# Kernel tuning notes

Hardware: AMD Instinct MI355X
Metric: run time of the kernel (lower is better)

## Reference

```python
import jax, jax.numpy as jnp
import numpy as np

P = 16  # patch side

def setup_inputs() -> dict:
    key = jax.random.key(0)
    k1, k2, k3, k4, k5 = jax.random.split(key, 5)
    B, H, W_img, C = 32, 512, 512, 3
    hidden = 256
    n = (H // P) * (W_img // P)
    x = jax.random.normal(k1, (B, H, W_img, C), dtype=jnp.float32)
    W = jax.random.normal(k2, (P * P * C, hidden), dtype=jnp.float32) * 0.02
    b = jax.random.normal(k3, (hidden,), dtype=jnp.float32) * 0.02
    cls_token = jax.random.normal(k4, (B, 1, hidden), dtype=jnp.float32)
    pos_embedding = jax.random.normal(k5, (B, n + 1, hidden), dtype=jnp.float32) * 0.02
    return {"x": x, "W": W, "b": b, "cls_token": cls_token, "pos_embedding": pos_embedding}

def _patchify(x):
    # (B,H,W,C) -> (B, n, P*P*C); patch index = col + (H/P)*row, flatten order (p,p,c)
    B, H, W_img, C = x.shape
    gh, gw = H // P, W_img // P
    x = x.reshape(B, gh, P, gw, P, C)
    x = x.transpose(0, 1, 3, 2, 4, 5)  # (B, gh, gw, P, P, C)
    return x.reshape(B, gh * gw, P * P * C)

def reference(x, W, b, cls_token, pos_embedding):
    patches = _patchify(x)                       # (B, n, P*P*C)
    proj = jnp.einsum('bnd,dh->bnh', patches, W) + b  # (B, n, hidden)
    out = jnp.concatenate([cls_token, proj], axis=1) + pos_embedding  # (B, n+1, hidden)
    return out
```

## Files before the change

kernel.cpp:

```cpp
#include <hip/hip_runtime.h>

#define PSZ 16
#define BATCH 32
#define IMGH 512
#define IMGW 512
#define CH 3
#define NPATCH 1024
#define M_TOT (BATCH*NPATCH)
#define K_TOT 768
#define N_TOT 256
#define ROWSTRIDE (IMGW*CH)
#define IMGSTRIDE (IMGH*IMGW*CH)

#define BM 64
#define BN 128
#define BK 64
#define KPAD 72
#define NKIT (K_TOT/BK)

typedef __bf16 bf16_t;
typedef bf16_t bf16x8 __attribute__((ext_vector_type(8)));
typedef bf16_t bf16x4 __attribute__((ext_vector_type(4)));
typedef float f32x4 __attribute__((ext_vector_type(4)));

__global__ void prep_w(const float* __restrict__ Wsrc,
                       bf16_t* __restrict__ wth, bf16_t* __restrict__ wtl) {
    __shared__ float tile[32][33];
    const int d0 = blockIdx.x * 32;
    const int h0 = blockIdx.y * 32;
    const int tid = threadIdx.x;
#pragma unroll
    for (int i = 0; i < 4; ++i) {
        int idx = tid + i * 256;
        int r = idx >> 5, c = idx & 31;
        tile[r][c] = Wsrc[(d0 + r) * N_TOT + h0 + c];
    }
    __syncthreads();
#pragma unroll
    for (int i = 0; i < 4; ++i) {
        int idx = tid + i * 256;
        int r = idx >> 5, c = idx & 31;
        float v = tile[c][r];
        bf16_t h = (bf16_t)v;
        bf16_t l = (bf16_t)(v - (float)h);
        size_t o = (size_t)(h0 + r) * K_TOT + d0 + c;
        wth[o] = h;
        wtl[o] = l;
    }
}

__global__ void cls_add(const float* __restrict__ cls, const float* __restrict__ pos,
                        float* __restrict__ out) {
    int i = blockIdx.x * 256 + threadIdx.x;
    int b = i >> 8, h = i & 255;
    size_t o = (size_t)b * (NPATCH + 1) * N_TOT + h;
    out[o] = cls[i] + pos[o];
}

__global__ __launch_bounds__(256, 2)
void patch_gemm(const float* __restrict__ x,
                const bf16_t* __restrict__ wth, const bf16_t* __restrict__ wtl,
                const float* __restrict__ bias, const float* __restrict__ pos,
                float* __restrict__ out) {
    __shared__ bf16_t Ah[BM * KPAD];
    __shared__ bf16_t Al[BM * KPAD];
    __shared__ bf16_t Bh[BN * KPAD];
    __shared__ bf16_t Bl[BN * KPAD];

    const int bid = blockIdx.x;
    const int xcd = bid & 7, kk = bid >> 3;
    const int t = xcd * 128 + kk;
    const int mtile = t >> 1;
    const int ntile = t & 1;

    const int tid = threadIdx.x;
    const int lane = tid & 63;
    const int wid = tid >> 6;
    const int wr = wid >> 1, wc = wid & 1;

    const int m0 = mtile * BM;
    const int n0 = ntile * BN;

    f32x4 acc[2][4] = {};

    const int l15 = lane & 15;
    const int kgrp = (lane >> 4) << 3;

    for (int kit = 0; kit < NKIT; ++kit) {
#pragma unroll
        for (int i = 0; i < 4; ++i) {
            int f = tid + i * 256;
            int row = f >> 4;
            int kl = (f & 15) << 2;
            int pm = m0 + row;
            int b = pm >> 10, pid = pm & 1023;
            int gr = pid >> 5, gc = pid & 31;
            int d = kit * BK + kl;
            int prow = d / 48;
            int poff = d % 48;
            const float* src = x + (size_t)b * IMGSTRIDE
                               + (gr * PSZ + prow) * ROWSTRIDE + gc * (PSZ * CH) + poff;
            float4 v = *(const float4*)src;
            bf16x4 hv, lv;
            hv[0] = (bf16_t)v.x; lv[0] = (bf16_t)(v.x - (float)hv[0]);
            hv[1] = (bf16_t)v.y; lv[1] = (bf16_t)(v.y - (float)hv[1]);
            hv[2] = (bf16_t)v.z; lv[2] = (bf16_t)(v.z - (float)hv[2]);
            hv[3] = (bf16_t)v.w; lv[3] = (bf16_t)(v.w - (float)hv[3]);
            int o = row * KPAD + kl;
            *reinterpret_cast<bf16x4*>(&Ah[o]) = hv;
            *reinterpret_cast<bf16x4*>(&Al[o]) = lv;
        }
#pragma unroll
        for (int i = 0; i < 4; ++i) {
            int f = tid + i * 256;
            int row = f >> 3;
            int kl = (f & 7) << 3;
            size_t g = (size_t)(n0 + row) * K_TOT + kit * BK + kl;
            int o = row * KPAD + kl;
            *reinterpret_cast<bf16x8*>(&Bh[o]) = *reinterpret_cast<const bf16x8*>(&wth[g]);
            *reinterpret_cast<bf16x8*>(&Bl[o]) = *reinterpret_cast<const bf16x8*>(&wtl[g]);
        }
        __syncthreads();

#pragma unroll
        for (int ks = 0; ks < 2; ++ks) {
            const int kb = ks * 32 + kgrp;
            bf16x8 afh[2], afl[2];
#pragma unroll
            for (int ar = 0; ar < 2; ++ar) {
                int o = (wr * 32 + ar * 16 + l15) * KPAD + kb;
                afh[ar] = *reinterpret_cast<const bf16x8*>(&Ah[o]);
                afl[ar] = *reinterpret_cast<const bf16x8*>(&Al[o]);
            }
            bf16x8 bfh[4], bfl[4];
#pragma unroll
            for (int bc = 0; bc < 4; ++bc) {
                int o = (wc * 64 + bc * 16 + l15) * KPAD + kb;
                bfh[bc] = *reinterpret_cast<const bf16x8*>(&Bh[o]);
                bfl[bc] = *reinterpret_cast<const bf16x8*>(&Bl[o]);
            }
#pragma unroll
            for (int ar = 0; ar < 2; ++ar)
#pragma unroll
                for (int bc = 0; bc < 4; ++bc) {
                    acc[ar][bc] = __builtin_amdgcn_mfma_f32_16x16x32_bf16(afh[ar], bfh[bc], acc[ar][bc], 0, 0, 0);
                    acc[ar][bc] = __builtin_amdgcn_mfma_f32_16x16x32_bf16(afh[ar], bfl[bc], acc[ar][bc], 0, 0, 0);
                    acc[ar][bc] = __builtin_amdgcn_mfma_f32_16x16x32_bf16(afl[ar], bfh[bc], acc[ar][bc], 0, 0, 0);
                }
        }
        __syncthreads();
    }

    const int colbase = n0 + wc * 64;
    float bvals[4];
#pragma unroll
    for (int bc = 0; bc < 4; ++bc) bvals[bc] = bias[colbase + bc * 16 + l15];

#pragma unroll
    for (int ar = 0; ar < 2; ++ar) {
        int rbase = m0 + wr * 32 + ar * 16 + ((lane >> 4) << 2);
#pragma unroll
        for (int j = 0; j < 4; ++j) {
            int pm = rbase + j;
            int b = pm >> 10, p = pm & 1023;
            size_t orow = (size_t)(b * (NPATCH + 1) + 1 + p) * N_TOT;
#pragma unroll
            for (int bc = 0; bc < 4; ++bc) {
                int col = colbase + bc * 16 + l15;
                out[orow + col] = acc[ar][bc][j] + bvals[bc] + pos[orow + col];
            }
        }
    }
}

extern "C" void kernel_launch(void* const* d_in, const int* in_sizes, int n_in,
                              void* d_out, int out_size, void* d_ws, size_t ws_size,
                              hipStream_t stream) {
    const float* x    = (const float*)d_in[0];
    const float* W    = (const float*)d_in[1];
    const float* bias = (const float*)d_in[2];
    const float* cls  = (const float*)d_in[3];
    const float* pos  = (const float*)d_in[4];
    float* out = (float*)d_out;

    bf16_t* wth = (bf16_t*)d_ws;
    bf16_t* wtl = wth + (size_t)K_TOT * N_TOT;

    prep_w<<<dim3(24, 8), 256, 0, stream>>>(W, wth, wtl);
    cls_add<<<32, 256, 0, stream>>>(cls, pos, out);
    patch_gemm<<<1024, 256, 0, stream>>>(x, wth, wtl, bias, pos, out);
}
```

Measured before the change: 210.2 us.

## Prepack weights in MFMA fragment order, double-buffer A tiles, drop B LDS staging

Weight prep now writes the hi/lo bf16 weights directly in the per-lane MFMA fragment order. The GEMM then loads B fragments straight from global memory (L2-resident) instead of staging them through shared memory. The A tile (patch pixels split into hi/lo bf16) is double-buffered in LDS, with the next tile's global loads issued before the MFMAs and the conversion stores after them, so there is one barrier per iteration. The smaller LDS footprint allows raising launch bounds to 4 blocks per CU. The trade-off is more global/L2 traffic for B, since each wave re-reads its fragments, plus some register pressure from the prefetched float4 values.

Measured after the change: 215.3 us. +2.4%, slower.

```diff
diff --git a/kernel.cpp b/kernel.cpp
--- a/kernel.cpp
+++ b/kernel.cpp
@@ -6,7 +6,6 @@
 #define IMGW 512
 #define CH 3
 #define NPATCH 1024
-#define M_TOT (BATCH*NPATCH)
 #define K_TOT 768
 #define N_TOT 256
 #define ROWSTRIDE (IMGW*CH)
@@ -20,33 +19,28 @@
 
 typedef __bf16 bf16_t;
 typedef bf16_t bf16x8 __attribute__((ext_vector_type(8)));
-typedef bf16_t bf16x4 __attribute__((ext_vector_type(4)));
 typedef float f32x4 __attribute__((ext_vector_type(4)));
 
 __global__ void prep_w(const float* __restrict__ Wsrc,
-                       bf16_t* __restrict__ wth, bf16_t* __restrict__ wtl) {
-    __shared__ float tile[32][33];
-    const int d0 = blockIdx.x * 32;
-    const int h0 = blockIdx.y * 32;
-    const int tid = threadIdx.x;
-#pragma unroll
-    for (int i = 0; i < 4; ++i) {
-        int idx = tid + i * 256;
-        int r = idx >> 5, c = idx & 31;
-        tile[r][c] = Wsrc[(d0 + r) * N_TOT + h0 + c];
-    }
-    __syncthreads();
-#pragma unroll
-    for (int i = 0; i < 4; ++i) {
-        int idx = tid + i * 256;
-        int r = idx >> 5, c = idx & 31;
-        float v = tile[c][r];
-        bf16_t h = (bf16_t)v;
-        bf16_t l = (bf16_t)(v - (float)h);
-        size_t o = (size_t)(h0 + r) * K_TOT + d0 + c;
-        wth[o] = h;
-        wtl[o] = l;
-    }
+                       bf16x8* __restrict__ wfh, bf16x8* __restrict__ wfl) {
+    int t = blockIdx.x * 256 + threadIdx.x;
+    int lane = t & 63;
+    int ks = (t >> 6) & 1;
+    int rest = t >> 7;
+    int kit = rest % 12;
+    int bcg = rest / 12;
+    int col = bcg * 16 + (lane & 15);
+    int kbase = kit * 64 + ks * 32 + ((lane >> 4) << 3);
+    bf16x8 h, l;
+#pragma unroll
+    for (int e = 0; e < 8; ++e) {
+        float v = Wsrc[(size_t)(kbase + e) * N_TOT + col];
+        bf16_t hh = (bf16_t)v;
+        h[e] = hh;
+        l[e] = (bf16_t)(v - (float)hh);
+    }
+    wfh[t] = h;
+    wfl[t] = l;
 }
 
 __global__ void cls_add(const float* __restrict__ cls, const float* __restrict__ pos,
@@ -57,19 +51,16 @@
     out[o] = cls[i] + pos[o];
 }
 
-__global__ __launch_bounds__(256, 2)
+__global__ __launch_bounds__(256, 4)
 void patch_gemm(const float* __restrict__ x,
-                const bf16_t* __restrict__ wth, const bf16_t* __restrict__ wtl,
+                const bf16x8* __restrict__ wfh, const bf16x8* __restrict__ wfl,
                 const float* __restrict__ bias, const float* __restrict__ pos,
                 float* __restrict__ out) {
-    __shared__ bf16_t Ah[BM * KPAD];
-    __shared__ bf16_t Al[BM * KPAD];
-    __shared__ bf16_t Bh[BN * KPAD];
-    __shared__ bf16_t Bl[BN * KPAD];
+    __shared__ bf16_t Ah[2][BM * KPAD];
+    __shared__ bf16_t Al[2][BM * KPAD];
 
     const int bid = blockIdx.x;
-    const int xcd = bid & 7, kk = bid >> 3;
-    const int t = xcd * 128 + kk;
+    const int t = (bid & 7) * 128 + (bid >> 3);
     const int mtile = t >> 1;
     const int ntile = t & 1;
 
@@ -85,59 +76,81 @@
 
     const int l15 = lane & 15;
     const int kgrp = (lane >> 4) << 3;
-
+    const int bcg0 = ntile * 8 + wc * 4;
+
+    const int rowb = tid >> 3;
+    const int kl8 = (tid & 7) << 3;
+    const float* srcbase[2];
+#pragma unroll
+    for (int i = 0; i < 2; ++i) {
+        int row = rowb + 32 * i;
+        int pm = m0 + row;
+        int b = pm >> 10, pid = pm & 1023;
+        int gr = pid >> 5, gc = pid & 31;
+        srcbase[i] = x + (size_t)b * IMGSTRIDE + (gr * PSZ) * ROWSTRIDE + gc * (PSZ * CH);
+    }
+
+#define LOADA(KIT, P0, P1, P2, P3)                                        \
+    {                                                                      \
+        int d = (KIT) * BK + kl8;                                          \
+        int prow = d / 48, poff = d % 48;                                  \
+        const float* s0 = srcbase[0] + prow * ROWSTRIDE + poff;            \
+        const float* s1 = srcbase[1] + prow * ROWSTRIDE + poff;            \
+        P0 = *(const float4*)s0;  P1 = *(const float4*)(s0 + 4);           \
+        P2 = *(const float4*)s1;  P3 = *(const float4*)(s1 + 4);           \
+    }
+
+#define CVTSTORE(BUF, P0, P1, P2, P3)                                      \
+    {                                                                      \
+        bf16x8 h, l;                                                       \
+        h[0]=(bf16_t)P0.x; l[0]=(bf16_t)(P0.x-(float)h[0]);                \
+        h[1]=(bf16_t)P0.y; l[1]=(bf16_t)(P0.y-(float)h[1]);                \
+        h[2]=(bf16_t)P0.z; l[2]=(bf16_t)(P0.z-(float)h[2]);                \
+        h[3]=(bf16_t)P0.w; l[3]=(bf16_t)(P0.w-(float)h[3]);                \
+        h[4]=(bf16_t)P1.x; l[4]=(bf16_t)(P1.x-(float)h[4]);                \
+        h[5]=(bf16_t)P1.y; l[5]=(bf16_t)(P1.y-(float)h[5]);                \
+        h[6]=(bf16_t)P1.z; l[6]=(bf16_t)(P1.z-(float)h[6]);                \
+        h[7]=(bf16_t)P1.w; l[7]=(bf16_t)(P1.w-(float)h[7]);                \
+        *reinterpret_cast<bf16x8*>(&Ah[BUF][rowb * KPAD + kl8]) = h;       \
+        *reinterpret_cast<bf16x8*>(&Al[BUF][rowb * KPAD + kl8]) = l;       \
+        h[0]=(bf16_t)P2.x; l[0]=(bf16_t)(P2.x-(float)h[0]);                \
+        h[1]=(bf16_t)P2.y; l[1]=(bf16_t)(P2.y-(float)h[1]);                \
+        h[2]=(bf16_t)P2.z; l[2]=(bf16_t)(P2.z-(float)h[2]);                \
+        h[3]=(bf16_t)P2.w; l[3]=(bf16_t)(P2.w-(float)h[3]);                \
+        h[4]=(bf16_t)P3.x; l[4]=(bf16_t)(P3.x-(float)h[4]);                \
+        h[5]=(bf16_t)P3.y; l[5]=(bf16_t)(P3.y-(float)h[5]);                \
+        h[6]=(bf16_t)P3.z; l[6]=(bf16_t)(P3.z-(float)h[6]);                \
+        h[7]=(bf16_t)P3.w; l[7]=(bf16_t)(P3.w-(float)h[7]);                \
+        *reinterpret_cast<bf16x8*>(&Ah[BUF][(rowb + 32) * KPAD + kl8]) = h;\
+        *reinterpret_cast<bf16x8*>(&Al[BUF][(rowb + 32) * KPAD + kl8]) = l;\
+    }
+
+    float4 p0, p1, p2, p3;
+    LOADA(0, p0, p1, p2, p3);
+    CVTSTORE(0, p0, p1, p2, p3);
+    __syncthreads();
+
+#pragma unroll 2
     for (int kit = 0; kit < NKIT; ++kit) {
-#pragma unroll
-        for (int i = 0; i < 4; ++i) {
-            int f = tid + i * 256;
-            int row = f >> 4;
-            int kl = (f & 15) << 2;
-            int pm = m0 + row;
-            int b = pm >> 10, pid = pm & 1023;
-            int gr = pid >> 5, gc = pid & 31;
-            int d = kit * BK + kl;
-            int prow = d / 48;
-            int poff = d % 48;
-            const float* src = x + (size_t)b * IMGSTRIDE
-                               + (gr * PSZ + prow) * ROWSTRIDE + gc * (PSZ * CH) + poff;
-            float4 v = *(const float4*)src;
-            bf16x4 hv, lv;
-            hv[0] = (bf16_t)v.x; lv[0] = (bf16_t)(v.x - (float)hv[0]);
-            hv[1] = (bf16_t)v.y; lv[1] = (bf16_t)(v.y - (float)hv[1]);
-            hv[2] = (bf16_t)v.z; lv[2] = (bf16_t)(v.z - (float)hv[2]);
-            hv[3] = (bf16_t)v.w; lv[3] = (bf16_t)(v.w - (float)hv[3]);
-            int o = row * KPAD + kl;
-            *reinterpret_cast<bf16x4*>(&Ah[o]) = hv;
-            *reinterpret_cast<bf16x4*>(&Al[o]) = lv;
-        }
-#pragma unroll
-        for (int i = 0; i < 4; ++i) {
-            int f = tid + i * 256;
-            int row = f >> 3;
-            int kl = (f & 7) << 3;
-            size_t g = (size_t)(n0 + row) * K_TOT + kit * BK + kl;
-            int o = row * KPAD + kl;
-            *reinterpret_cast<bf16x8*>(&Bh[o]) = *reinterpret_cast<const bf16x8*>(&wth[g]);
-            *reinterpret_cast<bf16x8*>(&Bl[o]) = *reinterpret_cast<const bf16x8*>(&wtl[g]);
-        }
-        __syncthreads();
+        const int cur = kit & 1;
+        if (kit < NKIT - 1) LOADA(kit + 1, p0, p1, p2, p3);
 
 #pragma unroll
         for (int ks = 0; ks < 2; ++ks) {
+            bf16x8 bfh[4], bfl[4];
+#pragma unroll
+            for (int bc = 0; bc < 4; ++bc) {
+                int idx = (((bcg0 + bc) * 12 + kit) * 2 + ks) * 64 + lane;
+                bfh[bc] = wfh[idx];
+                bfl[bc] = wfl[idx];
+            }
             const int kb = ks * 32 + kgrp;
             bf16x8 afh[2], afl[2];
 #pragma unroll
             for (int ar = 0; ar < 2; ++ar) {
                 int o = (wr * 32 + ar * 16 + l15) * KPAD + kb;
-                afh[ar] = *reinterpret_cast<const bf16x8*>(&Ah[o]);
-                afl[ar] = *reinterpret_cast<const bf16x8*>(&Al[o]);
-            }
-            bf16x8 bfh[4], bfl[4];
-#pragma unroll
-            for (int bc = 0; bc < 4; ++bc) {
-                int o = (wc * 64 + bc * 16 + l15) * KPAD + kb;
-                bfh[bc] = *reinterpret_cast<const bf16x8*>(&Bh[o]);
-                bfl[bc] = *reinterpret_cast<const bf16x8*>(&Bl[o]);
+                afh[ar] = *reinterpret_cast<const bf16x8*>(&Ah[cur][o]);
+                afl[ar] = *reinterpret_cast<const bf16x8*>(&Al[cur][o]);
             }
 #pragma unroll
             for (int ar = 0; ar < 2; ++ar)
@@ -148,6 +161,8 @@
                     acc[ar][bc] = __builtin_amdgcn_mfma_f32_16x16x32_bf16(afl[ar], bfh[bc], acc[ar][bc], 0, 0, 0);
                 }
         }
+
+        if (kit < NKIT - 1) CVTSTORE(cur ^ 1, p0, p1, p2, p3);
         __syncthreads();
     }
 
@@ -171,6 +186,8 @@
             }
         }
     }
+#undef LOADA
+#undef CVTSTORE
 }
 
 extern "C" void kernel_launch(void* const* d_in, const int* in_sizes, int n_in,
@@ -183,10 +200,10 @@
     const float* pos  = (const float*)d_in[4];
     float* out = (float*)d_out;
 
-    bf16_t* wth = (bf16_t*)d_ws;
-    bf16_t* wtl = wth + (size_t)K_TOT * N_TOT;
-
-    prep_w<<<dim3(24, 8), 256, 0, stream>>>(W, wth, wtl);
+    bf16x8* wfh = (bf16x8*)d_ws;
+    bf16x8* wfl = wfh + 24576;
+
+    prep_w<<<96, 256, 0, stream>>>(W, wfh, wfl);
     cls_add<<<32, 256, 0, stream>>>(cls, pos, out);
-    patch_gemm<<<1024, 256, 0, stream>>>(x, wth, wtl, bias, pos, out);
-}
+    patch_gemm<<<1024, 256, 0, stream>>>(x, wfh, wfl, bias, pos, out);
+}
```
